# Performance work log

Measured on AMD Instinct MI355X. Metric: run time of the kernel, lower is better.

The kernel has to match this reference:

```python
import jax, jax.numpy as jnp
import numpy as np


def setup_inputs() -> dict:
    key = jax.random.key(0)
    k1, k2 = jax.random.split(key)
    N, A, B, C = 512, 1024, 64, 16
    x = jax.random.normal(k1, (N, A), dtype=jnp.float32)
    T = jax.random.normal(k2, (A, B, C), dtype=jnp.float32)
    return {"x": x, "T": T}


def reference(x, T):
    # x: (N, A); T: (A, B, C)
    N = x.shape[0]
    A, B, C = T.shape
    # M_i = T * f(x_i)  -> (N, B, C)
    M = (x @ T.reshape(A, B * C)).reshape(N, B, C)
    # pairwise L1 distance over C: (N, N, B)
    l1 = jnp.abs(M[:, None, :, :] - M[None, :, :, :]).sum(axis=-1)
    # o(x_i)_b = sum_j exp(-||M_ib - M_jb||_1) ; subtract 1 for j == i term
    out = jnp.exp(-l1).sum(axis=1) - 1.0  # (N, B)
    return jnp.concatenate([x, out], axis=1)  # (N, A + B)
```

## Files before the change

kernel.cpp:

```cpp
#include <hip/hip_runtime.h>
#include <hip/hip_bf16.h>
#include <math.h>

#define N_   512
#define A_   1024
#define B_   64
#define C_   16
#define NBC  1024
#define OUTW 1088

#define NSCALE (-0.02254211681280365f)
#define Q8SCALE 0.6666667f
#define SCREEN 32u

typedef __attribute__((ext_vector_type(8))) short short8;
typedef __attribute__((ext_vector_type(4))) float floatx4;

__device__ __forceinline__ unsigned short f2bf_rne(float f) {
  union { float f; unsigned u; } v; v.f = f;
  unsigned r = v.u + 0x7FFFu + ((v.u >> 16) & 1u);
  return (unsigned short)(r >> 16);
}

#if __has_builtin(__builtin_amdgcn_exp2f)
__device__ __forceinline__ float exp2_hw(float x) { return __builtin_amdgcn_exp2f(x); }
#else
__device__ __forceinline__ float exp2_hw(float x) {
  float r; asm("v_exp_f32 %0, %1" : "=v"(r) : "v"(x)); return r;
}
#endif

#if __has_builtin(__builtin_amdgcn_sad_u16)
__device__ __forceinline__ unsigned sad16(unsigned a, unsigned b, unsigned c) {
  return __builtin_amdgcn_sad_u16(a, b, c);
}
#else
__device__ __forceinline__ unsigned sad16(unsigned a, unsigned b, unsigned c) {
  unsigned d; asm("v_sad_u16 %0, %1, %2, %3" : "=v"(d) : "v"(a), "v"(b), "v"(c));
  return d;
}
#endif

#if __has_builtin(__builtin_amdgcn_sad_u8)
__device__ __forceinline__ unsigned sad8(unsigned a, unsigned b, unsigned c) {
  return __builtin_amdgcn_sad_u8(a, b, c);
}
#else
__device__ __forceinline__ unsigned sad8(unsigned a, unsigned b, unsigned c) {
  unsigned d; asm("v_sad_u8 %0, %1, %2, %3" : "=v"(d) : "v"(a), "v"(b), "v"(c));
  return d;
}
#endif

__global__ __launch_bounds__(256) void prep_kernel(const float* __restrict__ x,
                                                   const float* __restrict__ W,
                                                   float* __restrict__ out,
                                                   unsigned short* __restrict__ xb,
                                                   unsigned short* __restrict__ wt) {
  __shared__ float tile[64][65];
  int bid = blockIdx.x, tid = threadIdx.x;
  if (bid < 136) {
    const float4* x4 = (const float4*)x;
    float4* out4 = (float4*)out;
    #pragma unroll
    for (int rep = 0; rep < 4; ++rep) {
      int idx = bid * 1024 + rep * 256 + tid;
      int row = idx / (OUTW / 4);
      int c4  = idx - row * (OUTW / 4);
      if (c4 < (A_ / 4)) {
        float4 f = x4[row * (A_ / 4) + c4];
        out4[idx] = f;
        ushort4 u;
        u.x = f2bf_rne(f.x); u.y = f2bf_rne(f.y);
        u.z = f2bf_rne(f.z); u.w = f2bf_rne(f.w);
        *(ushort4*)(xb + (size_t)row * A_ + c4 * 4) = u;
      } else {
        out4[idx] = make_float4(0.f, 0.f, 0.f, 0.f);
      }
    }
  } else {
    int tb = bid - 136;
    int k0 = (tb & 15) * 64, n0 = (tb >> 4) * 64;
    int tx = tid & 63, ty = tid >> 6;
    #pragma unroll
    for (int r = ty; r < 64; r += 4)
      tile[r][tx] = W[(k0 + r) * NBC + n0 + tx];
    __syncthreads();
    #pragma unroll
    for (int r = ty; r < 64; r += 4)
      wt[(size_t)(n0 + r) * A_ + k0 + tx] = f2bf_rne(tile[tx][r]);
  }
}

__global__ __launch_bounds__(64) void gemm_kernel(const unsigned short* __restrict__ xb,
                                                  const unsigned short* __restrict__ wt,
                                                  unsigned short* __restrict__ Mq,
                                                  unsigned char* __restrict__ Mq8) {
  int bid  = blockIdx.x;
  int m0   = (bid & 15) * 32;
  int n0   = (bid >> 4) * 32;
  int lane = threadIdx.x;
  int lo   = lane & 15;
  int quad = lane >> 4;

  const short8* pa0 = (const short8*)(xb + (size_t)(m0 + lo) * A_ + quad * 8);
  const short8* pa1 = (const short8*)(xb + (size_t)(m0 + 16 + lo) * A_ + quad * 8);
  const short8* pb0 = (const short8*)(wt + (size_t)(n0 + lo) * A_ + quad * 8);
  const short8* pb1 = (const short8*)(wt + (size_t)(n0 + 16 + lo) * A_ + quad * 8);

  floatx4 acc00 = {0.f, 0.f, 0.f, 0.f};
  floatx4 acc01 = acc00, acc10 = acc00, acc11 = acc00;

  #pragma unroll 4
  for (int ks = 0; ks < 32; ++ks) {
    short8 a0 = pa0[ks * 4];
    short8 a1 = pa1[ks * 4];
    short8 b0 = pb0[ks * 4];
    short8 b1 = pb1[ks * 4];
    acc00 = __builtin_amdgcn_mfma_f32_16x16x32_bf16(a0, b0, acc00, 0, 0, 0);
    acc01 = __builtin_amdgcn_mfma_f32_16x16x32_bf16(a0, b1, acc01, 0, 0, 0);
    acc10 = __builtin_amdgcn_mfma_f32_16x16x32_bf16(a1, b0, acc10, 0, 0, 0);
    acc11 = __builtin_amdgcn_mfma_f32_16x16x32_bf16(a1, b1, acc11, 0, 0, 0);
  }

  int b0i = n0 >> 4;
  #pragma unroll
  for (int r = 0; r < 4; ++r) {
    int row0 = m0 + quad * 4 + r;
    int row1 = row0 + 16;
    float a00 = acc00[r], a01 = acc01[r], a10 = acc10[r], a11 = acc11[r];
    Mq[(size_t)b0i * (N_ * C_)       + row0 * C_ + lo] = (unsigned short)(unsigned)fmaf(a00, 64.f, 32768.5f);
    Mq[(size_t)(b0i + 1) * (N_ * C_) + row0 * C_ + lo] = (unsigned short)(unsigned)fmaf(a01, 64.f, 32768.5f);
    Mq[(size_t)b0i * (N_ * C_)       + row1 * C_ + lo] = (unsigned short)(unsigned)fmaf(a10, 64.f, 32768.5f);
    Mq[(size_t)(b0i + 1) * (N_ * C_) + row1 * C_ + lo] = (unsigned short)(unsigned)fmaf(a11, 64.f, 32768.5f);
    Mq8[(size_t)b0i * (N_ * C_)       + row0 * C_ + lo] = (unsigned char)(unsigned)fminf(fmaxf(fmaf(a00, Q8SCALE, 128.5f), 0.f), 255.f);
    Mq8[(size_t)(b0i + 1) * (N_ * C_) + row0 * C_ + lo] = (unsigned char)(unsigned)fminf(fmaxf(fmaf(a01, Q8SCALE, 128.5f), 0.f), 255.f);
    Mq8[(size_t)b0i * (N_ * C_)       + row1 * C_ + lo] = (unsigned char)(unsigned)fminf(fmaxf(fmaf(a10, Q8SCALE, 128.5f), 0.f), 255.f);
    Mq8[(size_t)(b0i + 1) * (N_ * C_) + row1 * C_ + lo] = (unsigned char)(unsigned)fminf(fmaxf(fmaf(a11, Q8SCALE, 128.5f), 0.f), 255.f);
  }
}

__global__ __launch_bounds__(256) void pairwise_kernel(const unsigned char* __restrict__ Mq8,
                                                       const unsigned short* __restrict__ Mq,
                                                       float* __restrict__ out) {
  int b   = blockIdx.x;
  int it  = blockIdx.y;
  int tid = threadIdx.x;

  __shared__ uint4 smj[512];

  const uint4* Mb8 = (const uint4*)(Mq8 + (size_t)b * (N_ * C_));
  int il = tid & 31;
  int js = tid >> 5;
  int i  = it * 32 + il;

  uint4 ra = Mb8[i];

  #pragma unroll
  for (int idx = tid; idx < 512; idx += 256)
    smj[idx] = Mb8[idx];
  __syncthreads();

  int j0 = js * 64;
  #pragma unroll 4
  for (int jj = 0; jj < 64; ++jj) {
    uint4 q = smj[j0 + jj];
    unsigned s = sad8(ra.x, q.x, sad8(ra.y, q.y, 0u))
               + sad8(ra.z, q.z, sad8(ra.w, q.w, 0u));
    if (s - 1u < SCREEN) {
      int j = j0 + jj;
      const uint4* pi = (const uint4*)(Mq + (size_t)b * (N_ * C_) + i * C_);
      const uint4* pj = (const uint4*)(Mq + (size_t)b * (N_ * C_) + j * C_);
      uint4 xa = pi[0], xb2 = pi[1], ya = pj[0], yb = pj[1];
      unsigned t0 = sad16(xa.x, ya.x, 0u), t1 = sad16(xb2.x, yb.x, 0u);
      t0 = sad16(xa.y, ya.y, t0);  t1 = sad16(xb2.y, yb.y, t1);
      t0 = sad16(xa.z, ya.z, t0);  t1 = sad16(xb2.z, yb.z, t1);
      t0 = sad16(xa.w, ya.w, t0);  t1 = sad16(xb2.w, yb.w, t1);
      atomicAdd(&out[(size_t)i * OUTW + A_ + b], exp2_hw((float)(t0 + t1) * NSCALE));
    }
  }
}

extern "C" void kernel_launch(void* const* d_in, const int* in_sizes, int n_in,
                              void* d_out, int out_size, void* d_ws, size_t ws_size,
                              hipStream_t stream) {
  const float* x = (const float*)d_in[0];
  const float* T = (const float*)d_in[1];
  float* out = (float*)d_out;

  char* ws = (char*)d_ws;
  unsigned short* xb  = (unsigned short*)(ws);
  unsigned short* wt  = (unsigned short*)(ws + (1u << 20));
  unsigned short* Mq  = (unsigned short*)(ws + (3u << 20));
  unsigned char*  Mq8 = (unsigned char*)(ws + (4u << 20));

  prep_kernel<<<dim3(392), dim3(256), 0, stream>>>(x, T, out, xb, wt);
  gemm_kernel<<<dim3(512), dim3(64), 0, stream>>>(xb, wt, Mq, Mq8);
  pairwise_kernel<<<dim3(64, 16), dim3(256), 0, stream>>>(Mq8, Mq, out);
}
```

Baseline: 80.83 us.

## Restructure GEMM into 4-wave blocks and move output-column zeroing into GEMM

```diff
diff --git a/kernel.cpp b/kernel.cpp
--- a/kernel.cpp
+++ b/kernel.cpp
@@ -59,27 +59,22 @@
                                                    unsigned short* __restrict__ wt) {
   __shared__ float tile[64][65];
   int bid = blockIdx.x, tid = threadIdx.x;
-  if (bid < 136) {
+  if (bid < 128) {
     const float4* x4 = (const float4*)x;
     float4* out4 = (float4*)out;
     #pragma unroll
     for (int rep = 0; rep < 4; ++rep) {
       int idx = bid * 1024 + rep * 256 + tid;
-      int row = idx / (OUTW / 4);
-      int c4  = idx - row * (OUTW / 4);
-      if (c4 < (A_ / 4)) {
-        float4 f = x4[row * (A_ / 4) + c4];
-        out4[idx] = f;
-        ushort4 u;
-        u.x = f2bf_rne(f.x); u.y = f2bf_rne(f.y);
-        u.z = f2bf_rne(f.z); u.w = f2bf_rne(f.w);
-        *(ushort4*)(xb + (size_t)row * A_ + c4 * 4) = u;
-      } else {
-        out4[idx] = make_float4(0.f, 0.f, 0.f, 0.f);
-      }
+      int row = idx >> 8, c4 = idx & 255;
+      float4 f = x4[idx];
+      out4[row * (OUTW / 4) + c4] = f;
+      ushort4 u;
+      u.x = f2bf_rne(f.x); u.y = f2bf_rne(f.y);
+      u.z = f2bf_rne(f.z); u.w = f2bf_rne(f.w);
+      *(ushort4*)(xb + (size_t)idx * 4) = u;
     }
   } else {
-    int tb = bid - 136;
+    int tb = bid - 128;
     int k0 = (tb & 15) * 64, n0 = (tb >> 4) * 64;
     int tx = tid & 63, ty = tid >> 6;
     #pragma unroll
@@ -92,51 +87,51 @@
   }
 }
 
-__global__ __launch_bounds__(64) void gemm_kernel(const unsigned short* __restrict__ xb,
-                                                  const unsigned short* __restrict__ wt,
-                                                  unsigned short* __restrict__ Mq,
-                                                  unsigned char* __restrict__ Mq8) {
+__global__ __launch_bounds__(256) void gemm_kernel(const unsigned short* __restrict__ xb,
+                                                   const unsigned short* __restrict__ wt,
+                                                   unsigned short* __restrict__ Mq,
+                                                   unsigned char* __restrict__ Mq8,
+                                                   float* __restrict__ out) {
   int bid  = blockIdx.x;
-  int m0   = (bid & 15) * 32;
-  int n0   = (bid >> 4) * 32;
-  int lane = threadIdx.x;
+  int m0   = (bid & 7) * 64;
+  int n0   = (bid >> 3) * 32;
+  int tid  = threadIdx.x;
+  int w    = tid >> 6;
+  int lane = tid & 63;
   int lo   = lane & 15;
   int quad = lane >> 4;
+  int mw   = m0 + w * 16;
 
-  const short8* pa0 = (const short8*)(xb + (size_t)(m0 + lo) * A_ + quad * 8);
-  const short8* pa1 = (const short8*)(xb + (size_t)(m0 + 16 + lo) * A_ + quad * 8);
+  const short8* pa  = (const short8*)(xb + (size_t)(mw + lo) * A_ + quad * 8);
   const short8* pb0 = (const short8*)(wt + (size_t)(n0 + lo) * A_ + quad * 8);
   const short8* pb1 = (const short8*)(wt + (size_t)(n0 + 16 + lo) * A_ + quad * 8);
 
-  floatx4 acc00 = {0.f, 0.f, 0.f, 0.f};
-  floatx4 acc01 = acc00, acc10 = acc00, acc11 = acc00;
+  floatx4 acc0 = {0.f, 0.f, 0.f, 0.f};
+  floatx4 acc1 = acc0;
 
-  #pragma unroll 4
+  #pragma unroll 8
   for (int ks = 0; ks < 32; ++ks) {
-    short8 a0 = pa0[ks * 4];
-    short8 a1 = pa1[ks * 4];
+    short8 a  = pa[ks * 4];
     short8 b0 = pb0[ks * 4];
     short8 b1 = pb1[ks * 4];
-    acc00 = __builtin_amdgcn_mfma_f32_16x16x32_bf16(a0, b0, acc00, 0, 0, 0);
-    acc01 = __builtin_amdgcn_mfma_f32_16x16x32_bf16(a0, b1, acc01, 0, 0, 0);
-    acc10 = __builtin_amdgcn_mfma_f32_16x16x32_bf16(a1, b0, acc10, 0, 0, 0);
-    acc11 = __builtin_amdgcn_mfma_f32_16x16x32_bf16(a1, b1, acc11, 0, 0, 0);
+    acc0 = __builtin_amdgcn_mfma_f32_16x16x32_bf16(a, b0, acc0, 0, 0, 0);
+    acc1 = __builtin_amdgcn_mfma_f32_16x16x32_bf16(a, b1, acc1, 0, 0, 0);
+  }
+
+  if (tid < 128) {
+    int idx = bid * 128 + tid;
+    out[(size_t)(idx >> 6) * OUTW + A_ + (idx & 63)] = 0.f;
   }
 
   int b0i = n0 >> 4;
   #pragma unroll
   for (int r = 0; r < 4; ++r) {
-    int row0 = m0 + quad * 4 + r;
-    int row1 = row0 + 16;
-    float a00 = acc00[r], a01 = acc01[r], a10 = acc10[r], a11 = acc11[r];
-    Mq[(size_t)b0i * (N_ * C_)       + row0 * C_ + lo] = (unsigned short)(unsigned)fmaf(a00, 64.f, 32768.5f);
-    Mq[(size_t)(b0i + 1) * (N_ * C_) + row0 * C_ + lo] = (unsigned short)(unsigned)fmaf(a01, 64.f, 32768.5f);
-    Mq[(size_t)b0i * (N_ * C_)       + row1 * C_ + lo] = (unsigned short)(unsigned)fmaf(a10, 64.f, 32768.5f);
-    Mq[(size_t)(b0i + 1) * (N_ * C_) + row1 * C_ + lo] = (unsigned short)(unsigned)fmaf(a11, 64.f, 32768.5f);
-    Mq8[(size_t)b0i * (N_ * C_)       + row0 * C_ + lo] = (unsigned char)(unsigned)fminf(fmaxf(fmaf(a00, Q8SCALE, 128.5f), 0.f), 255.f);
-    Mq8[(size_t)(b0i + 1) * (N_ * C_) + row0 * C_ + lo] = (unsigned char)(unsigned)fminf(fmaxf(fmaf(a01, Q8SCALE, 128.5f), 0.f), 255.f);
-    Mq8[(size_t)b0i * (N_ * C_)       + row1 * C_ + lo] = (unsigned char)(unsigned)fminf(fmaxf(fmaf(a10, Q8SCALE, 128.5f), 0.f), 255.f);
-    Mq8[(size_t)(b0i + 1) * (N_ * C_) + row1 * C_ + lo] = (unsigned char)(unsigned)fminf(fmaxf(fmaf(a11, Q8SCALE, 128.5f), 0.f), 255.f);
+    int row = mw + quad * 4 + r;
+    float a0 = acc0[r], a1 = acc1[r];
+    Mq[(size_t)b0i * (N_ * C_)       + row * C_ + lo] = (unsigned short)(unsigned)fmaf(a0, 64.f, 32768.5f);
+    Mq[(size_t)(b0i + 1) * (N_ * C_) + row * C_ + lo] = (unsigned short)(unsigned)fmaf(a1, 64.f, 32768.5f);
+    Mq8[(size_t)b0i * (N_ * C_)       + row * C_ + lo] = (unsigned char)(unsigned)fminf(fmaxf(fmaf(a0, Q8SCALE, 128.5f), 0.f), 255.f);
+    Mq8[(size_t)(b0i + 1) * (N_ * C_) + row * C_ + lo] = (unsigned char)(unsigned)fminf(fmaxf(fmaf(a1, Q8SCALE, 128.5f), 0.f), 255.f);
   }
 }
 
@@ -194,7 +189,7 @@
   unsigned short* Mq  = (unsigned short*)(ws + (3u << 20));
   unsigned char*  Mq8 = (unsigned char*)(ws + (4u << 20));
 
-  prep_kernel<<<dim3(392), dim3(256), 0, stream>>>(x, T, out, xb, wt);
-  gemm_kernel<<<dim3(512), dim3(64), 0, stream>>>(xb, wt, Mq, Mq8);
+  prep_kernel<<<dim3(384), dim3(256), 0, stream>>>(x, T, out, xb, wt);
+  gemm_kernel<<<dim3(256), dim3(256), 0, stream>>>(xb, wt, Mq, Mq8, out);
   pairwise_kernel<<<dim3(64, 16), dim3(256), 0, stream>>>(Mq8, Mq, out);
 }
```

After: 85.09 us. +5.3%, slower.
